# Kernel optimization log

Measured on AMD Instinct MI355X. Metric: run time of the kernel, lower is better.

Reference implementation:

```python
import jax, jax.numpy as jnp
import numpy as np

SR = 22050.0  # samplerate; nyquist = SR/2


def _conv1d(x, w, b, pad):
    # x: [B, Cin, T], w: [Cout, Cin, K]
    y = jax.lax.conv_general_dilated(x, w, (1,), [(pad, pad)],
                                     dimension_numbers=('NCH', 'OIH', 'NCH'))
    return y + b[None, :, None]


def _lrelu(x):
    return jnp.where(x >= 0, x, 0.2 * x)


def _lin_upsample(x, factor):
    # torch F.upsample(mode='linear', align_corners=False) ~ half-pixel linear resize
    B, C, T = x.shape
    return jax.image.resize(x, (B, C, T * factor), method='linear')


def _oscillator_bank(f, a, sr):
    # f, a: [B, n_osc, T] -> audio [B, T]
    f = jnp.clip(f, 20.0, sr / 2.0)
    phase = jnp.cumsum(f * (2.0 * np.pi / sr), axis=-1)  # cumulative phase integration
    return jnp.sum(jnp.sin(phase) * a, axis=1)


def _noise_bank2(mags, noise):
    # mags: [B, n_coeffs, n_frames] rfft magnitudes per frame; noise: [B, total_samples]
    B, n_coeffs, n_frames = mags.shape
    window = (n_coeffs - 1) * 2
    hop = window // 2
    total = hop * n_frames
    padded = jnp.pad(noise, ((0, 0), (0, hop)))           # [B, total + hop]
    blocks = padded.reshape(B, n_frames + 1, hop)
    frames = jnp.concatenate([blocks[:, :-1], blocks[:, 1:]], axis=-1)  # [B, n_frames, window]
    spec = jnp.fft.rfft(frames, axis=-1)                   # [B, n_frames, n_coeffs]
    spec = spec * mags.transpose(0, 2, 1)                  # filter white noise per frame
    filt = jnp.fft.irfft(spec, n=window, axis=-1)          # (torch normalized rfft/irfft scales cancel)
    out = jnp.zeros((B, hop * (n_frames + 1)), filt.dtype)
    out = out.at[:, :n_frames * hop].add(filt[..., :hop].reshape(B, -1))
    out = out.at[:, hop:].add(filt[..., hop:].reshape(B, -1))
    return out[:, :total].reshape(B, 1, total)


def _forward(x, noise, mw0, mb0, mw1, mb1, mw2, mb2, mw3, mb3, fw, fb,
             gw0, gb0, gw1, gb1, gw2, gb2, gw3, gb3, lw, lb,
             nw0, nb0, nw1, nb1, nw2, nb2, nw3, nb3, nlw, nlb):
    B, _, T = x.shape
    up = noise.shape[1] // T  # upsample_factor = output_size // input_size
    n_osc = fw.shape[0]

    # oscillator frequency ranges (constants, as in __init__)
    stops = np.geomspace(20.0, SR / 2.0, num=n_osc)
    diffs = np.diff(np.concatenate([[0.0], stops]))
    starts = jnp.asarray(stops - diffs, jnp.float32)[None, :, None]
    diffs_j = jnp.asarray(diffs, jnp.float32)[None, :, None]

    # loudness path (main2 -> loudness ** 2)
    h = x
    for w_, b_ in ((gw0, gb0), (gw1, gb1), (gw2, gb2), (gw3, gb3)):
        h = _lrelu(_conv1d(h, w_, b_, 1))
    loud = _conv1d(h, lw, lb, 1) ** 2  # [B, n_osc, T]

    # frequency path (main -> sigmoid -> map to [start, stop])
    h = x
    for w_, b_ in ((mw0, mb0), (mw1, mb1), (mw2, mb2), (mw3, mb3)):
        h = _lrelu(_conv1d(h, w_, b_, 1))
    f = starts + jax.nn.sigmoid(_conv1d(h, fw, fb, 1)) * diffs_j  # [B, n_osc, T]

    h = x
    for w_, b_ in ((nw0, nb0), (nw1, nb1), (nw2, nb2), (nw3, nb3)):
        h = jnp.repeat(h, 2, axis=-1)
        h = _lrelu(_conv1d(h, w_, b_, 3))
    n_l = _conv1d(h, nlw, nlb, 1) ** 2  # [B, 17, 1024]

    loud = _lin_upsample(loud, up)  # [B, n_osc, output_size]
    f = _lin_upsample(f, up)
    harmonic = _oscillator_bank(f, loud, SR).reshape(B, 1, -1)
    return harmonic + _noise_bank2(n_l, noise)


def setup_inputs() -> dict:
    key = jax.random.key(0)
    ks = jax.random.split(key, 40)
    B, Cin, T, c, n_osc, out_size = 16, 128, 64, 512, 128, 16384
    n_coeffs = out_size // 1024 + 1  # 17
    inp = {}
    inp['x'] = jax.random.normal(ks[0], (B, Cin, T), jnp.float32)
    inp['noise'] = jax.random.uniform(ks[1], (B, out_size), jnp.float32, minval=-1.0, maxval=1.0)
    specs = [('mw0', c, Cin, 3), ('mw1', c, c, 3), ('mw2', c, c, 3), ('mw3', c, c, 3), ('fw', n_osc, c, 3),
             ('gw0', c, Cin, 3), ('gw1', c, c, 3), ('gw2', c, c, 3), ('gw3', c, c, 3), ('lw', n_osc, c, 3),
             ('nw0', c, Cin, 7), ('nw1', c, c, 7), ('nw2', c, c, 7), ('nw3', c, c, 7), ('nlw', n_coeffs, c, 3)]
    for j, (nm, o, i, ksz) in enumerate(specs):
        kw, kb = jax.random.split(ks[2 + j])
        inp[nm] = jax.random.normal(kw, (o, i, ksz), jnp.float32) * (1.0 / np.sqrt(i * ksz))
        inp[nm.replace('w', 'b', 1)] = jax.random.normal(kb, (o,), jnp.float32) * 0.01
    return inp


def reference(x, noise, mw0, mb0, mw1, mb1, mw2, mb2, mw3, mb3, fw, fb,
              gw0, gb0, gw1, gb1, gw2, gb2, gw3, gb3, lw, lb,
              nw0, nb0, nw1, nb1, nw2, nb2, nw3, nb3, nlw, nlb):
    return _forward(x, noise, mw0, mb0, mw1, mb1, mw2, mb2, mw3, mb3, fw, fb,
                    gw0, gb0, gw1, gb1, gw2, gb2, gw3, gb3, lw, lb,
                    nw0, nb0, nw1, nb1, nw2, nb2, nw3, nb3, nlw, nlb)
```

## Files before the change

### kernel.cpp

```cpp
#include <hip/hip_runtime.h>
#include <math.h>

#define ACT_LRELU  0
#define ACT_SIGMAP 1
#define ACT_SQUARE 2

typedef __attribute__((ext_vector_type(8))) short v8s;
typedef __attribute__((ext_vector_type(4))) short v4s;
typedef __attribute__((ext_vector_type(16))) float f32x16;

static __device__ __forceinline__ float lrelu(float x) { return x >= 0.f ? x : 0.2f * x; }

static __device__ __forceinline__ short bf16rne(float x) {
  unsigned u = __float_as_uint(x);
  unsigned r = (u + 0x7FFFu + ((u >> 16) & 1u)) >> 16;
  return (short)r;
}
static __device__ __forceinline__ float bf16tof(short h) {
  return __uint_as_float(((unsigned)(unsigned short)h) << 16);
}
static __device__ __forceinline__ void split3(float v, short& h, short& l, short& q) {
  h = bf16rne(v); float r1 = v - bf16tof(h);
  l = bf16rne(r1); float r2 = r1 - bf16tof(l);
  q = bf16rne(r2);
}

__global__ void __launch_bounds__(256) prep_acts(
    const float* __restrict__ x, short* __restrict__ xm3)
{
  int e = blockIdx.x * 256 + threadIdx.x;
  if (e >= 131072) return;
  int b = e >> 13, rem = e & 8191, t = rem >> 7, ci = rem & 127;
  float v = x[((size_t)(b * 128) + ci) * 64 + t];
  short h, l, q; split3(v, h, l, q);
  size_t o = ((size_t)(b * 64) + t) * 128 + ci;
  xm3[0 * 131072 + o] = h;
  xm3[1 * 131072 + o] = l;
  xm3[2 * 131072 + o] = q;
}

__global__ void __launch_bounds__(256) prep_panels(
    const float* mw0, const float* mw1, const float* mw2, const float* mw3, const float* fw,
    const float* gw0, const float* gw1, const float* gw2, const float* gw3, const float* lw,
    short* __restrict__ mP, short* __restrict__ gP)
{
  int i = blockIdx.x * 256 + threadIdx.x;
  const int PER = 114688;
  if (i >= 2 * PER) return;
  int path = i >= PER ? 1 : 0;
  int r = i - path * PER;
  int layer, Cin, Cout; size_t poff;
  if (r < 8192)        { layer = 0;              Cin = 128; Cout = 512; poff = 0; }
  else if (r < 40960)  { layer = 1; r -= 8192;   Cin = 512; Cout = 512; poff = 589824; }
  else if (r < 73728)  { layer = 2; r -= 40960;  Cin = 512; Cout = 512; poff = 2949120; }
  else if (r < 106496) { layer = 3; r -= 73728;  Cin = 512; Cout = 512; poff = 5308416; }
  else                 { layer = 4; r -= 106496; Cin = 512; Cout = 128; poff = 7667712; }
  const float* Wm[5] = {mw0, mw1, mw2, mw3, fw};
  const float* Wg[5] = {gw0, gw1, gw2, gw3, lw};
  const float* W = path ? Wg[layer] : Wm[layer];
  short* P = (path ? gP : mP) + poff;
  const int nci8 = Cin >> 3;
  int co = r / nci8, ci = (r - co * nci8) * 8;
  const int K3 = 3 * Cin;
  const float* wp = W + (size_t)(co * Cin + ci) * 3;
  v8s hv[3], lv[3], qv[3];
#pragma unroll
  for (int j = 0; j < 8; ++j)
#pragma unroll
    for (int tap = 0; tap < 3; ++tap) {
      short h, l, q; split3(wp[j * 3 + tap], h, l, q);
      hv[tap][j] = h; lv[tap][j] = l; qv[tap][j] = q;
    }
#pragma unroll
  for (int tap = 0; tap < 3; ++tap) {
    size_t base = (size_t)co * K3 + tap * Cin + ci;
    *(v8s*)&P[(size_t)0 * Cout * K3 + base] = hv[tap];
    *(v8s*)&P[(size_t)1 * Cout * K3 + base] = lv[tap];
    *(v8s*)&P[(size_t)2 * Cout * K3 + base] = qv[tap];
  }
}

__global__ void __launch_bounds__(128, 2) conv_path_tap(
    const short* __restrict__ actM, const short* __restrict__ actG,
    const short* __restrict__ Pm, const short* __restrict__ Pg,
    float* __restrict__ partial, int Cin, int Cout, int psIn)
{
  const int mtiles = Cout >> 6;
  const int nblk = 2 * mtiles * 16 * 3;
  const int Q = nblk >> 3;
  int d = blockIdx.x;
  int idx = (d & 7) * Q + (d >> 3);
  int mt = idx % mtiles; int r = idx / mtiles;
  int nt = r & 15; r >>= 4;
  int tap = r % 3; int path = r / 3;

  const short* act = path ? actG : actM;
  const short* P   = path ? Pg : Pm;
  const int K3 = 3 * Cin;
  const int co0 = mt * 64;
  const int NT  = Cin >> 5;
  const int npl = path ? 2 : 3;

  const int tid = threadIdx.x;
  const int w = tid >> 6;
  const int l = tid & 63;

  __shared__ __align__(16) short Al[3][64 * 40];
  __shared__ __align__(16) short Bl[3][64 * 40];

  f32x16 acc[2] = {};
  v8s rA[3][2], rB[3][2];

  auto LOADA = [&](int t) {
    int ci0 = t << 5;
#pragma unroll
    for (int pl = 0; pl < 3; ++pl) {
      if (pl >= npl) break;
#pragma unroll
      for (int it = 0; it < 2; ++it) {
        int e = it * 128 + tid;
        int row = e >> 2, c8 = e & 3;
        rA[pl][it] = *(const v8s*)&P[(size_t)pl * Cout * K3 + (size_t)(co0 + row) * K3
                                     + tap * Cin + ci0 + c8 * 8];
      }
    }
  };
  auto LOADB = [&](int t) {
    int ci0 = t << 5;
#pragma unroll
    for (int pl = 0; pl < 3; ++pl) {
      if (pl >= npl) break;
#pragma unroll
      for (int it = 0; it < 2; ++it) {
        int e = it * 128 + tid;
        int n = e >> 2, c8 = e & 3;
        int trow = n + tap - 1;
        v8s vv = {};
        if (trow >= 0 && trow < 64)
          vv = *(const v8s*)&act[(size_t)pl * psIn + ((size_t)(nt * 64 + trow)) * Cin
                                 + ci0 + c8 * 8];
        rB[pl][it] = vv;
      }
    }
  };
  auto WRITE = [&]() {
#pragma unroll
    for (int pl = 0; pl < 3; ++pl) {
      if (pl >= npl) break;
#pragma unroll
      for (int it = 0; it < 2; ++it) {
        int e = it * 128 + tid;
        *(v8s*)&Al[pl][(e >> 2) * 40 + (e & 3) * 8] = rA[pl][it];
        *(v8s*)&Bl[pl][(e >> 2) * 40 + (e & 3) * 8] = rB[pl][it];
      }
    }
  };

  LOADA(0); LOADB(0);
  WRITE();
  __syncthreads();

  for (int t = 0; t < NT; ++t) {
    if (t + 1 < NT) { LOADA(t + 1); LOADB(t + 1); }
    const int lr = l & 31, lh = (l >> 5) * 8;
#pragma unroll
    for (int kk = 0; kk < 2; ++kk) {
      const int ao = (w * 32 + lr) * 40 + kk * 16 + lh;
      v8s a0 = *(const v8s*)&Al[0][ao];
      v8s a1 = *(const v8s*)&Al[1][ao];
#pragma unroll
      for (int fn = 0; fn < 2; ++fn) {
        const int bo = (fn * 32 + lr) * 40 + kk * 16 + lh;
        v8s b0 = *(const v8s*)&Bl[0][bo];
        v8s b1 = *(const v8s*)&Bl[1][bo];
        acc[fn] = __builtin_amdgcn_mfma_f32_32x32x16_bf16(a0, b0, acc[fn], 0, 0, 0);
        acc[fn] = __builtin_amdgcn_mfma_f32_32x32x16_bf16(a0, b1, acc[fn], 0, 0, 0);
        acc[fn] = __builtin_amdgcn_mfma_f32_32x32x16_bf16(a1, b0, acc[fn], 0, 0, 0);
        if (path == 0) {
          v8s a2 = *(const v8s*)&Al[2][ao];
          v8s b2 = *(const v8s*)&Bl[2][bo];
          acc[fn] = __builtin_amdgcn_mfma_f32_32x32x16_bf16(a1, b1, acc[fn], 0, 0, 0);
          acc[fn] = __builtin_amdgcn_mfma_f32_32x32x16_bf16(a0, b2, acc[fn], 0, 0, 0);
          acc[fn] = __builtin_amdgcn_mfma_f32_32x32x16_bf16(a2, b0, acc[fn], 0, 0, 0);
        }
      }
    }
    __syncthreads();
    if (t + 1 < NT) { WRITE(); __syncthreads(); }
  }

  const int hi4 = 4 * (l >> 5);
  const size_t pbase = (size_t)(tap * 2 + path) * 1024;
#pragma unroll
  for (int fn = 0; fn < 2; ++fn) {
    int gn = nt * 64 + fn * 32 + (l & 31);
#pragma unroll
    for (int q4 = 0; q4 < 4; ++q4) {
      int co = co0 + w * 32 + q4 * 8 + hi4;
      float4 v = {acc[fn][q4 * 4 + 0], acc[fn][q4 * 4 + 1],
                  acc[fn][q4 * 4 + 2], acc[fn][q4 * 4 + 3]};
      *(float4*)&partial[(pbase + gn) * Cout + co] = v;
    }
  }
}

__global__ void __launch_bounds__(256) finalize_lrelu(
    const float* __restrict__ partial,
    const float* __restrict__ BsM, const float* __restrict__ BsG,
    short* __restrict__ soutM, short* __restrict__ soutG)
{
  int e = blockIdx.x * 256 + threadIdx.x;
  int c4 = e & 127, gn = (e >> 7) & 1023, path = e >> 17;
  const float* Bs = path ? BsG : BsM;
  short* sout = path ? soutG : soutM;
  size_t base = ((size_t)(path) * 1024 + gn) * 512 + c4 * 4;
  const size_t TS = (size_t)2 * 1024 * 512;
  float4 s0 = *(const float4*)&partial[base];
  float4 s1 = *(const float4*)&partial[base + TS];
  float4 s2 = *(const float4*)&partial[base + 2 * TS];
  float4 bi = *(const float4*)&Bs[c4 * 4];
  const float* p0 = &s0.x; const float* p1 = &s1.x;
  const float* p2 = &s2.x; const float* pb = &bi.x;
  v4s h4, l4, q4v;
#pragma unroll
  for (int j = 0; j < 4; ++j) {
    float z = lrelu(p0[j] + p1[j] + p2[j] + pb[j]);
    short h, lo, qq; split3(z, h, lo, qq);
    h4[j] = h; l4[j] = lo; q4v[j] = qq;
  }
  size_t o = (size_t)gn * 512 + c4 * 4;
  *(v4s*)&sout[0 * 524288 + o] = h4;
  *(v4s*)&sout[1 * 524288 + o] = l4;
  *(v4s*)&sout[2 * 524288 + o] = q4v;
}

__global__ void __launch_bounds__(256) finalize_l5(
    const float* __restrict__ partial,
    const float* __restrict__ fb, const float* __restrict__ lb,
    float* __restrict__ fsm, float* __restrict__ lsm)
{
  __shared__ float bandS[2][128];
  int tid = threadIdx.x;
  if (tid < 128) {
    double lg = log(551.25);
    double stop  = 20.0 * exp(lg * (double)tid / 127.0);
    double start = (tid == 0) ? 0.0 : 20.0 * exp(lg * (double)(tid - 1) / 127.0);
    bandS[0][tid] = (float)start;
    bandS[1][tid] = (float)(stop - start);
  }
  __syncthreads();

  int e = blockIdx.x * 256 + tid;
  int c4 = e & 31, gn = (e >> 5) & 1023, path = e >> 15;
  size_t base = ((size_t)(path) * 1024 + gn) * 128 + c4 * 4;
  const size_t TS = (size_t)2 * 1024 * 128;
  float4 s0 = *(const float4*)&partial[base];
  float4 s1 = *(const float4*)&partial[base + TS];
  float4 s2 = *(const float4*)&partial[base + 2 * TS];
  float4 bi = *(const float4*)&((path ? lb : fb)[c4 * 4]);
  const float* p0 = &s0.x; const float* p1 = &s1.x;
  const float* p2 = &s2.x; const float* pb = &bi.x;
  int b = gn >> 6, t = gn & 63;
#pragma unroll
  for (int j = 0; j < 4; ++j) {
    int co = c4 * 4 + j;
    float z = p0[j] + p1[j] + p2[j] + pb[j];
    if (path == 0)
      fsm[((size_t)(b * 128) + co) * 64 + t] = bandS[0][co] + bandS[1][co] / (1.f + expf(-z));
    else
      lsm[((size_t)(b * 128) + co) * 64 + t] = z * z;
  }
}

__global__ void __launch_bounds__(256) fold_all(
    const float* __restrict__ nw0, const float* __restrict__ nw1,
    const float* __restrict__ nw2, const float* __restrict__ nw3,
    const float* __restrict__ nlw,
    short* __restrict__ E1, short* __restrict__ E2,
    short* __restrict__ E3, short* __restrict__ E4,
    short* __restrict__ Pnl)
{
  int i = blockIdx.x * 256 + threadIdx.x;
  if (i >= 106496) {
    if (i >= 108544) return;
    int idx = i - 106496;
    int co = idx >> 6, ci = (idx & 63) * 8;
    v8s hv[3], lv[3];
#pragma unroll
    for (int j = 0; j < 8; ++j)
#pragma unroll
      for (int tap = 0; tap < 3; ++tap) {
        float v = (co < 17) ? nlw[((size_t)(co * 512 + ci + j)) * 3 + tap] : 0.f;
        short h = bf16rne(v);
        hv[tap][j] = h;
        lv[tap][j] = bf16rne(v - bf16tof(h));
      }
#pragma unroll
    for (int tap = 0; tap < 3; ++tap) {
      *(v8s*)&Pnl[(size_t)(0 * 32 + co) * 1536 + tap * 512 + ci] = hv[tap];
      *(v8s*)&Pnl[(size_t)(1 * 32 + co) * 1536 + tap * 512 + ci] = lv[tap];
    }
    return;
  }
  const float* W; short* Ag; int Cin; int idx;
  if (i < 8192)        { W = nw0; Ag = E1; Cin = 128; idx = i; }
  else if (i < 40960)  { W = nw1; Ag = E2; Cin = 512; idx = i - 8192; }
  else if (i < 73728)  { W = nw2; Ag = E3; Cin = 512; idx = i - 40960; }
  else                 { W = nw3; Ag = E4; Cin = 512; idx = i - 73728; }
  const int nci8 = Cin >> 3;
  int co = idx / nci8, ci = (idx - co * nci8) * 8;
  const float* wp = W + (size_t)(co * Cin + ci) * 7;
  const int K = Cin * 4;
  v8s he[4], le[4], ho[4], lo4[4];
#pragma unroll
  for (int j = 0; j < 8; ++j) {
    const float* w = wp + j * 7;
    float fe[4] = {w[0],        w[1] + w[2], w[3] + w[4], w[5] + w[6]};
    float fo[4] = {w[0] + w[1], w[2] + w[3], w[4] + w[5], w[6]};
#pragma unroll
    for (int q = 0; q < 4; ++q) {
      short h1 = bf16rne(fe[q]);
      he[q][j] = h1; le[q][j] = bf16rne(fe[q] - bf16tof(h1));
      short h2 = bf16rne(fo[q]);
      ho[q][j] = h2; lo4[q][j] = bf16rne(fo[q] - bf16tof(h2));
    }
  }
#pragma unroll
  for (int q = 0; q < 4; ++q) {
    size_t kbase = (size_t)q * Cin + ci;
    *(v8s*)&Ag[((size_t)(0 * 512 + co)) * K + kbase] = he[q];
    *(v8s*)&Ag[((size_t)(1 * 512 + co)) * K + kbase] = le[q];
    *(v8s*)&Ag[((size_t)(2 * 512 + co)) * K + kbase] = ho[q];
    *(v8s*)&Ag[((size_t)(3 * 512 + co)) * K + kbase] = lo4[q];
  }
}

template<int MF, int BNS, int CIN>
__global__ void __launch_bounds__(256, 2) conv_noise(
    const short* __restrict__ actIn, const short* __restrict__ Ag,
    const float* __restrict__ Bs, short* __restrict__ actOut,
    int Sin, int psIn, int psOut)
{
  constexpr int NF   = BNS / 64;
  constexpr int BM   = MF * 64;
  constexpr int AITS = BM / 32;
  constexpr int BITS = BNS / 32;
  constexpr int K    = CIN * 4;
  constexpr int nci  = CIN / 64;
  constexpr int NT   = 4 * nci;
  const int mtiles = 512 / BM;
  const int stiles = Sin / BNS;
  const int nblk = mtiles * 2 * 16 * stiles;
  const int Q = nblk >> 3;
  int d = blockIdx.x;
  int idx = (d & 7) * Q + (d >> 3);
  int mt = idx % mtiles;
  int t1 = idx / mtiles;
  int par = t1 & 1;
  int rest = t1 >> 1;
  int st = rest % stiles;
  int b = rest / stiles;

  const int co0 = mt * BM;
  const int s0 = st * BNS;
  const int soff = par ? -1 : -2;

  const int tid = threadIdx.x;
  const int w = tid >> 6, wm = w & 1, wn = w >> 1;
  const int l = tid & 63;

  __shared__ __align__(16) short Al[2][BM * 72];
  __shared__ __align__(16) short Bl[2][BNS * 72];

  f32x16 acc[MF][NF] = {};
  v8s rA[2][AITS], rB[2][BITS];

  auto LOADA = [&](int t) {
    int q = t / nci, ci0 = (t % nci) << 6;
#pragma unroll
    for (int pl = 0; pl < 2; ++pl)
#pragma unroll
      for (int it = 0; it < AITS; ++it) {
        int e = it * 256 + tid;
        int row = e >> 3, c8 = e & 7;
        rA[pl][it] = *(const v8s*)&Ag[((size_t)((par * 2 + pl) * 512 + co0 + row)) * K
                                      + q * CIN + ci0 + c8 * 8];
      }
  };
  auto LOADB = [&](int t) {
    int q = t / nci, ci0 = (t % nci) << 6;
#pragma unroll
    for (int pl = 0; pl < 2; ++pl)
#pragma unroll
      for (int it = 0; it < BITS; ++it) {
        int e = it * 256 + tid;
        int n = e >> 3, c8 = e & 7;
        int srow = s0 + n + q + soff;
        v8s vv = {};
        if (srow >= 0 && srow < Sin)
          vv = *(const v8s*)&actIn[(size_t)pl * psIn + ((size_t)(b * Sin + srow)) * CIN
                                   + ci0 + c8 * 8];
        rB[pl][it] = vv;
      }
  };
  auto WRITE = [&]() {
#pragma unroll
    for (int pl = 0; pl < 2; ++pl) {
#pragma unroll
      for (int it = 0; it < AITS; ++it) {
        int e = it * 256 + tid;
        *(v8s*)&Al[pl][(e >> 3) * 72 + (e & 7) * 8] = rA[pl][it];
      }
#pragma unroll
      for (int it = 0; it < BITS; ++it) {
        int e = it * 256 + tid;
        *(v8s*)&Bl[pl][(e >> 3) * 72 + (e & 7) * 8] = rB[pl][it];
      }
    }
  };

  LOADA(0); LOADB(0);
  WRITE();
  __syncthreads();

  for (int t = 0; t < NT; ++t) {
    if (t + 1 < NT) { LOADA(t + 1); LOADB(t + 1); }
    const int lr = l & 31, lh = (l >> 5) * 8;
#pragma unroll
    for (int kk = 0; kk < 4; ++kk) {
      v8s ah[MF], al[MF], bh[NF], bl[NF];
#pragma unroll
      for (int fm = 0; fm < MF; ++fm) {
        int ab = (wm * (MF * 32) + fm * 32 + lr) * 72 + kk * 16 + lh;
        ah[fm] = *(const v8s*)&Al[0][ab];
        al[fm] = *(const v8s*)&Al[1][ab];
      }
#pragma unroll
      for (int fn = 0; fn < NF; ++fn) {
        int bb = (wn * (BNS / 2) + fn * 32 + lr) * 72 + kk * 16 + lh;
        bh[fn] = *(const v8s*)&Bl[0][bb];
        bl[fn] = *(const v8s*)&Bl[1][bb];
      }
#pragma unroll
      for (int fm = 0; fm < MF; ++fm)
#pragma unroll
        for (int fn = 0; fn < NF; ++fn) {
          acc[fm][fn] = __builtin_amdgcn_mfma_f32_32x32x16_bf16(ah[fm], bh[fn], acc[fm][fn], 0, 0, 0);
          acc[fm][fn] = __builtin_amdgcn_mfma_f32_32x32x16_bf16(ah[fm], bl[fn], acc[fm][fn], 0, 0, 0);
          acc[fm][fn] = __builtin_amdgcn_mfma_f32_32x32x16_bf16(al[fm], bh[fn], acc[fm][fn], 0, 0, 0);
        }
    }
    __syncthreads();
    if (t + 1 < NT) { WRITE(); __syncthreads(); }
  }

  const int hi4 = 4 * (l >> 5);
  const int T2 = 2 * Sin;
#pragma unroll
  for (int fm = 0; fm < MF; ++fm)
#pragma unroll
    for (int q4 = 0; q4 < 4; ++q4) {
      int co = co0 + wm * (MF * 32) + fm * 32 + q4 * 8 + hi4;
      float4 bia = *(const float4*)&Bs[co];
      const float* bp = &bia.x;
#pragma unroll
      for (int fn = 0; fn < NF; ++fn) {
        int s_l = wn * (BNS / 2) + fn * 32 + (l & 31);
        int t = 2 * (s0 + s_l) + par;
        v4s h4, l4;
#pragma unroll
        for (int j = 0; j < 4; ++j) {
          float z = lrelu(acc[fm][fn][q4 * 4 + j] + bp[j]);
          short h = bf16rne(z);
          h4[j] = h;
          l4[j] = bf16rne(z - bf16tof(h));
        }
        size_t o = ((size_t)(b * T2) + t) * 512 + co;
        *(v4s*)&actOut[0 * (size_t)psOut + o] = h4;
        *(v4s*)&actOut[1 * (size_t)psOut + o] = l4;
      }
    }
}

#define NL_PS4 8388608

__global__ void __launch_bounds__(128) conv_nl_mfma(
    const short* __restrict__ act, const short* __restrict__ Pnl,
    const float* __restrict__ Bs, float* __restrict__ outNl)
{
  const int bid = blockIdx.x;
  const int b = bid >> 4, t0 = (bid & 15) << 6;
  const int tid = threadIdx.x;
  const int w = tid >> 6;
  const int l = tid & 63;

  __shared__ __align__(16) short Al[2 * 3 * 32 * 72];
  __shared__ __align__(16) short Bl[2 * 66 * 72];

  f32x16 acc = {};

  for (int ci0 = 0; ci0 < 512; ci0 += 64) {
    for (int e = tid; e < 1536; e += 128) {
      int c8 = e & 7, row = e >> 3;
      int pl = row >= 96;
      int r2 = row - pl * 96;
      int tap = r2 >> 5, co = r2 & 31;
      v8s vv = *(const v8s*)&Pnl[(size_t)(pl * 32 + co) * 1536 + tap * 512 + ci0 + c8 * 8];
      *(v8s*)&Al[row * 72 + c8 * 8] = vv;
    }
    for (int e = tid; e < 1056; e += 128) {
      int c8 = e & 7, r = (e >> 3) % 66, pl = (e >> 3) / 66;
      int t = t0 + r - 1;
      v8s vv = {};
      if (t >= 0 && t < 1024)
        vv = *(const v8s*)&act[(size_t)pl * NL_PS4 + ((size_t)(b << 10) + t) * 512 + ci0 + c8 * 8];
      *(v8s*)&Bl[(pl * 66 + r) * 72 + c8 * 8] = vv;
    }
    __syncthreads();
    const int lr = l & 31, lh = (l >> 5) * 8;
#pragma unroll
    for (int kk = 0; kk < 4; ++kk)
#pragma unroll
      for (int tap = 0; tap < 3; ++tap) {
        v8s a_h = *(const v8s*)&Al[((0 * 3 + tap) * 32 + lr) * 72 + kk * 16 + lh];
        v8s a_l = *(const v8s*)&Al[((1 * 3 + tap) * 32 + lr) * 72 + kk * 16 + lh];
        int brow = w * 32 + lr + tap;
        v8s b_h = *(const v8s*)&Bl[(0 * 66 + brow) * 72 + kk * 16 + lh];
        v8s b_l = *(const v8s*)&Bl[(1 * 66 + brow) * 72 + kk * 16 + lh];
        acc = __builtin_amdgcn_mfma_f32_32x32x16_bf16(a_h, b_h, acc, 0, 0, 0);
        acc = __builtin_amdgcn_mfma_f32_32x32x16_bf16(a_h, b_l, acc, 0, 0, 0);
        acc = __builtin_amdgcn_mfma_f32_32x32x16_bf16(a_l, b_h, acc, 0, 0, 0);
      }
    __syncthreads();
  }

  const int t = t0 + w * 32 + (l & 31);
  const int hi4 = 4 * (l >> 5);
#pragma unroll
  for (int q4 = 0; q4 < 4; ++q4) {
#pragma unroll
    for (int j = 0; j < 4; ++j) {
      int co = q4 * 8 + hi4 + j;
      if (co < 17) {
        float z = acc[q4 * 4 + j] + Bs[co];
        outNl[((size_t)(b * 17) + co) * 1024 + t] = z * z;
      }
    }
  }
}

__global__ void __launch_bounds__(64) noise_filter(
    const float* __restrict__ noise, const float* __restrict__ mags,
    float* __restrict__ filt)
{
  __shared__ float ct[32], st[32];
  int tid = threadIdx.x;
  if (tid < 32) {
    double a = (double)tid * (3.14159265358979323846 / 16.0);
    ct[tid] = (float)cos(a);
    st[tid] = (float)sin(a);
  }
  __syncthreads();

  int fidx = blockIdx.x * 64 + tid;
  int b = fidx >> 10, i = fidx & 1023;

  float xv[32];
#pragma unroll
  for (int n = 0; n < 32; ++n) {
    int idx = i * 16 + n;
    xv[n] = (idx < 16384) ? noise[(size_t)b * 16384 + idx] : 0.f;
  }

  float Yr[17], Yi[17];
#pragma unroll
  for (int k = 0; k <= 16; ++k) {
    float xr = 0.f, xi = 0.f;
    int kk = 0;
#pragma unroll
    for (int n = 0; n < 32; ++n) {
      xr += xv[n] * ct[kk];
      xi -= xv[n] * st[kk];
      kk = (kk + k) & 31;
    }
    float m = mags[((size_t)b * 17 + k) * 1024 + i];
    Yr[k] = xr * m;
    Yi[k] = xi * m;
  }

  float* fo = filt + ((size_t)b * 1024 + i) * 32;
#pragma unroll
  for (int n = 0; n < 32; ++n) {
    float v = Yr[0] + ((n & 1) ? -Yr[16] : Yr[16]);
    int kk = n;
#pragma unroll
    for (int k = 1; k <= 15; ++k) {
      v += 2.f * (Yr[k] * ct[kk] - Yi[k] * st[kk]);
      kk = (kk + n) & 31;
    }
    fo[n] = v * (1.f / 32.f);
  }
}

static __device__ __forceinline__ int clamp64(int i) { return i < 0 ? 0 : (i > 63 ? 63 : i); }

__global__ void __launch_bounds__(256) osc_phase(
    const float* __restrict__ fsm, double* __restrict__ phaseBase)
{
  const int o = blockIdx.x, b = blockIdx.y;
  const float* frow = fsm + (size_t)(b * 128 + o) * 64;
  const int c = threadIdx.x;

  const float ic0 = ((float)(c * 64) - 127.5f) * (1.0f / 256.0f);
  const int ilo = (int)floorf(ic0);
  float f0 = frow[clamp64(ilo)], f1 = frow[clamp64(ilo + 1)], f2 = frow[clamp64(ilo + 2)];

  double local = 0.0;
#pragma unroll 8
  for (int j = 0; j < 64; ++j) {
    float ic = ic0 + (float)j * (1.0f / 256.0f);
    float fl = floorf(ic);
    float w  = ic - fl;
    bool hi = ((int)fl) > ilo;
    float fa = hi ? f1 : f0;
    float fb = hi ? f2 : f1;
    float f = fa * (1.f - w) + fb * w;
    f = fminf(fmaxf(f, 20.f), 11025.f);
    local += (double)f;
  }
  local *= (1.0 / 22050.0);

  __shared__ double ps[256];
  ps[c] = local;
  __syncthreads();
  for (int off = 1; off < 256; off <<= 1) {
    double v = (c >= off) ? ps[c - off] : 0.0;
    __syncthreads();
    ps[c] += v;
    __syncthreads();
  }
  phaseBase[(size_t)(b * 128 + o) * 256 + c] = ps[c] - local;
}

__global__ void __launch_bounds__(128) osc_sum(
    const float* __restrict__ fsm, const float* __restrict__ lsm,
    const double* __restrict__ phaseBase, const float* __restrict__ filt,
    float* __restrict__ out)
{
  const int c = blockIdx.x, b = blockIdx.y;
  const int tid = threadIdx.x;
  __shared__ float contrib[128][65];
  __shared__ float part[2][64];
  const int o = tid;
  const float* frow = fsm + (size_t)(b * 128 + o) * 64;
  const float* arow = lsm + (size_t)(b * 128 + o) * 64;

  double pb = phaseBase[(size_t)(b * 128 + o) * 256 + c];
  float fb0 = (float)(pb - floor(pb));

  const float ic0 = ((float)(c * 64) - 127.5f) * (1.0f / 256.0f);
  const int ilo = (int)floorf(ic0);
  float f0 = frow[clamp64(ilo)], f1 = frow[clamp64(ilo + 1)], f2 = frow[clamp64(ilo + 2)];
  float a0 = arow[clamp64(ilo)], a1 = arow[clamp64(ilo + 1)], a2 = arow[clamp64(ilo + 2)];

  float rel = 0.f, comp = 0.f;
#pragma unroll 8
  for (int j = 0; j < 64; ++j) {
    float ic = ic0 + (float)j * (1.0f / 256.0f);
    float fl = floorf(ic);
    float w  = ic - fl;
    bool hi = ((int)fl) > ilo;
    float fa = hi ? f1 : f0;
    float fb = hi ? f2 : f1;
    float f = fa * (1.f - w) + fb * w;
    f = fminf(fmaxf(f, 20.f), 11025.f);
    float y = f * (1.0f / 22050.0f) - comp;
    float t = rel + y;
    comp = (t - rel) - y;
    rel = t;
    float tot = fb0 + rel;
    float frac = tot - floorf(tot);
    float s = sinpif(2.f * frac);
    float aa = hi ? a1 : a0;
    float ab = hi ? a2 : a1;
    float am = aa * (1.f - w) + ab * w;
    contrib[o][j] = s * am;
  }
  __syncthreads();
  int half = tid >> 6, tl = tid & 63;
  float sum = 0.f;
  for (int oo = 0; oo < 64; ++oo) sum += contrib[half * 64 + oo][tl];
  part[half][tl] = sum;
  __syncthreads();
  if (tid < 64) {
    int t = c * 64 + tid;
    float v = part[0][tid] + part[1][tid];
    int i0 = t >> 4, r = t & 15;
    v += filt[((size_t)(b << 10) + i0) * 32 + r];
    if (i0 > 0) v += filt[((size_t)(b << 10) + i0 - 1) * 32 + 16 + r];
    out[(size_t)b * 16384 + t] = v;
  }
}

extern "C" void kernel_launch(void* const* d_in, const int* in_sizes, int n_in,
                              void* d_out, int out_size, void* d_ws, size_t ws_size,
                              hipStream_t stream)
{
  (void)in_sizes; (void)n_in; (void)out_size; (void)ws_size;

  const float* x     = (const float*)d_in[0];
  const float* noise = (const float*)d_in[1];
  const float* mw0 = (const float*)d_in[2];  const float* mb0 = (const float*)d_in[3];
  const float* mw1 = (const float*)d_in[4];  const float* mb1 = (const float*)d_in[5];
  const float* mw2 = (const float*)d_in[6];  const float* mb2 = (const float*)d_in[7];
  const float* mw3 = (const float*)d_in[8];  const float* mb3 = (const float*)d_in[9];
  const float* fw  = (const float*)d_in[10]; const float* fb  = (const float*)d_in[11];
  const float* gw0 = (const float*)d_in[12]; const float* gb0 = (const float*)d_in[13];
  const float* gw1 = (const float*)d_in[14]; const float* gb1 = (const float*)d_in[15];
  const float* gw2 = (const float*)d_in[16]; const float* gb2 = (const float*)d_in[17];
  const float* gw3 = (const float*)d_in[18]; const float* gb3 = (const float*)d_in[19];
  const float* lw  = (const float*)d_in[20]; const float* lb  = (const float*)d_in[21];
  const float* nw0 = (const float*)d_in[22]; const float* nb0 = (const float*)d_in[23];
  const float* nw1 = (const float*)d_in[24]; const float* nb1 = (const float*)d_in[25];
  const float* nw2 = (const float*)d_in[26]; const float* nb2 = (const float*)d_in[27];
  const float* nw3 = (const float*)d_in[28]; const float* nb3 = (const float*)d_in[29];
  const float* nlw = (const float*)d_in[30]; const float* nlb = (const float*)d_in[31];

  char* W8 = (char*)d_ws;
  short* mP  = (short*)(W8 + 0);
  short* gP  = (short*)(W8 + 16515072);
  short* hm0 = (short*)(W8 + 33030144);
  short* hm1 = (short*)(W8 + 36175872);
  short* hg0 = (short*)(W8 + 39321600);
  short* hg1 = (short*)(W8 + 42467328);
  float* partial = (float*)(W8 + 45613056);
  short* xm3 = (short*)(W8 + 58720256);
  float* fsm = (float*)(W8 + 59506688);
  float* lsm = (float*)(W8 + 60030976);
  short* Pnl = (short*)(W8 + 60555264);

  short* E4  = (short*)(W8 + 0);
  short* E3  = (short*)(W8 + 33554432);
  short* E2  = (short*)(W8 + 41943040);
  short* E1  = (short*)(W8 + 50331648);
  short* l1out = (short*)(W8 + 52428800);
  short* l2out = (short*)(W8 + 25165824);
  short* l3out = (short*)(W8 + 8388608);
  short* l4act = (short*)(W8 + 25165824);

  float* nl   = (float*)(W8 + 0);
  float* filt = (float*)(W8 + 1114112);
  double* phaseBase = (double*)(W8 + 4194304);

  float* out = (float*)d_out;

  const int PS_X = 131072;
  const int PS_H = 524288;

  prep_acts<<<512, 256, 0, stream>>>(x, xm3);
  prep_panels<<<896, 256, 0, stream>>>(mw0, mw1, mw2, mw3, fw,
                                       gw0, gw1, gw2, gw3, lw, mP, gP);

  conv_path_tap<<<768, 128, 0, stream>>>(xm3, xm3, mP + 0, gP + 0, partial, 128, 512, PS_X);
  finalize_lrelu<<<1024, 256, 0, stream>>>(partial, mb0, gb0, hm0, hg0);
  conv_path_tap<<<768, 128, 0, stream>>>(hm0, hg0, mP + 589824, gP + 589824, partial, 512, 512, PS_H);
  finalize_lrelu<<<1024, 256, 0, stream>>>(partial, mb1, gb1, hm1, hg1);
  conv_path_tap<<<768, 128, 0, stream>>>(hm1, hg1, mP + 2949120, gP + 2949120, partial, 512, 512, PS_H);
  finalize_lrelu<<<1024, 256, 0, stream>>>(partial, mb2, gb2, hm0, hg0);
  conv_path_tap<<<768, 128, 0, stream>>>(hm0, hg0, mP + 5308416, gP + 5308416, partial, 512, 512, PS_H);
  finalize_lrelu<<<1024, 256, 0, stream>>>(partial, mb3, gb3, hm1, hg1);
  conv_path_tap<<<192, 128, 0, stream>>>(hm1, hg1, mP + 7667712, gP + 7667712, partial, 512, 128, PS_H);
  finalize_l5<<<256, 256, 0, stream>>>(partial, fb, lb, fsm, lsm);

  fold_all<<<424, 256, 0, stream>>>(nw0, nw1, nw2, nw3, nlw, E1, E2, E3, E4, Pnl);
  conv_noise<1, 64, 128><<<256, 256, 0, stream>>>(xm3, E1, nb0, l1out, 64, PS_X, 1048576);
  conv_noise<2, 64, 512><<<256, 256, 0, stream>>>(l1out, E2, nb1, l2out, 128, 1048576, 2097152);
  conv_noise<2, 128, 512><<<256, 256, 0, stream>>>(l2out, E3, nb2, l3out, 256, 2097152, 4194304);
  conv_noise<2, 128, 512><<<512, 256, 0, stream>>>(l3out, E4, nb3, l4act, 512, 4194304, 8388608);

  conv_nl_mfma<<<256, 128, 0, stream>>>(l4act, Pnl, nlb, nl);

  noise_filter<<<256, 64, 0, stream>>>(noise, nl, filt);

  osc_phase<<<dim3(128, 16), 256, 0, stream>>>(fsm, phaseBase);
  osc_sum<<<dim3(256, 16), 128, 0, stream>>>(fsm, lsm, phaseBase, filt, out);
}
```

Measured before the change: 535.7 us.

## Reuse shifted activation slab across taps in conv_noise and fuse noise filter

conv_noise now loads one activation slab of BNS+3 rows per 64-channel chunk and reuses it for all four taps by offsetting the LDS row index, instead of reloading the B tile for every tap. This cuts global loads and LDS writes for the activation operand. In exchange, A-panel loads are pipelined per tap, and extra branches are added on the last tap. Separately, the noise-layer conv is fused with the per-frame FFT filter, so magnitudes stay in shared memory instead of round-tripping through global memory, though only half the threads do the filter work. The conv_path_tap loop guards are also rewritten from break to if.

```diff
diff --git a/kernel.cpp b/kernel.cpp
--- a/kernel.cpp
+++ b/kernel.cpp
@@ -114,46 +114,43 @@
   auto LOADA = [&](int t) {
     int ci0 = t << 5;
 #pragma unroll
-    for (int pl = 0; pl < 3; ++pl) {
-      if (pl >= npl) break;
-#pragma unroll
-      for (int it = 0; it < 2; ++it) {
-        int e = it * 128 + tid;
-        int row = e >> 2, c8 = e & 3;
-        rA[pl][it] = *(const v8s*)&P[(size_t)pl * Cout * K3 + (size_t)(co0 + row) * K3
-                                     + tap * Cin + ci0 + c8 * 8];
-      }
-    }
+    for (int pl = 0; pl < 3; ++pl)
+      if (pl < npl)
+#pragma unroll
+        for (int it = 0; it < 2; ++it) {
+          int e = it * 128 + tid;
+          int row = e >> 2, c8 = e & 3;
+          rA[pl][it] = *(const v8s*)&P[(size_t)pl * Cout * K3 + (size_t)(co0 + row) * K3
+                                       + tap * Cin + ci0 + c8 * 8];
+        }
   };
   auto LOADB = [&](int t) {
     int ci0 = t << 5;
 #pragma unroll
-    for (int pl = 0; pl < 3; ++pl) {
-      if (pl >= npl) break;
-#pragma unroll
-      for (int it = 0; it < 2; ++it) {
-        int e = it * 128 + tid;
-        int n = e >> 2, c8 = e & 3;
-        int trow = n + tap - 1;
-        v8s vv = {};
-        if (trow >= 0 && trow < 64)
-          vv = *(const v8s*)&act[(size_t)pl * psIn + ((size_t)(nt * 64 + trow)) * Cin
-                                 + ci0 + c8 * 8];
-        rB[pl][it] = vv;
-      }
-    }
+    for (int pl = 0; pl < 3; ++pl)
+      if (pl < npl)
+#pragma unroll
+        for (int it = 0; it < 2; ++it) {
+          int e = it * 128 + tid;
+          int n = e >> 2, c8 = e & 3;
+          int trow = n + tap - 1;
+          v8s vv = {};
+          if (trow >= 0 && trow < 64)
+            vv = *(const v8s*)&act[(size_t)pl * psIn + ((size_t)(nt * 64 + trow)) * Cin
+                                   + ci0 + c8 * 8];
+          rB[pl][it] = vv;
+        }
   };
   auto WRITE = [&]() {
 #pragma unroll
-    for (int pl = 0; pl < 3; ++pl) {
-      if (pl >= npl) break;
-#pragma unroll
-      for (int it = 0; it < 2; ++it) {
-        int e = it * 128 + tid;
-        *(v8s*)&Al[pl][(e >> 2) * 40 + (e & 3) * 8] = rA[pl][it];
-        *(v8s*)&Bl[pl][(e >> 2) * 40 + (e & 3) * 8] = rB[pl][it];
-      }
-    }
+    for (int pl = 0; pl < 3; ++pl)
+      if (pl < npl)
+#pragma unroll
+        for (int it = 0; it < 2; ++it) {
+          int e = it * 128 + tid;
+          *(v8s*)&Al[pl][(e >> 2) * 40 + (e & 3) * 8] = rA[pl][it];
+          *(v8s*)&Bl[pl][(e >> 2) * 40 + (e & 3) * 8] = rB[pl][it];
+        }
   };
 
   LOADA(0); LOADB(0);
@@ -344,10 +341,10 @@
   constexpr int NF   = BNS / 64;
   constexpr int BM   = MF * 64;
   constexpr int AITS = BM / 32;
-  constexpr int BITS = BNS / 32;
+  constexpr int SLAB = BNS + 3;
+  constexpr int BSL  = (2 * SLAB * 8 + 255) / 256;
   constexpr int K    = CIN * 4;
   constexpr int nci  = CIN / 64;
-  constexpr int NT   = 4 * nci;
   const int mtiles = 512 / BM;
   const int stiles = Sin / BNS;
   const int nblk = mtiles * 2 * 16 * stiles;
@@ -370,13 +367,13 @@
   const int l = tid & 63;
 
   __shared__ __align__(16) short Al[2][BM * 72];
-  __shared__ __align__(16) short Bl[2][BNS * 72];
+  __shared__ __align__(16) short Bl[2][SLAB * 72];
 
   f32x16 acc[MF][NF] = {};
-  v8s rA[2][AITS], rB[2][BITS];
-
-  auto LOADA = [&](int t) {
-    int q = t / nci, ci0 = (t % nci) << 6;
+  v8s rA[2][AITS];
+  v8s rBS[BSL];
+
+  auto LOADA = [&](int q, int ci0) {
 #pragma unroll
     for (int pl = 0; pl < 2; ++pl)
 #pragma unroll
@@ -387,71 +384,88 @@
                                       + q * CIN + ci0 + c8 * 8];
       }
   };
-  auto LOADB = [&](int t) {
-    int q = t / nci, ci0 = (t % nci) << 6;
+  auto WRITEA = [&]() {
 #pragma unroll
     for (int pl = 0; pl < 2; ++pl)
 #pragma unroll
-      for (int it = 0; it < BITS; ++it) {
+      for (int it = 0; it < AITS; ++it) {
         int e = it * 256 + tid;
-        int n = e >> 3, c8 = e & 7;
-        int srow = s0 + n + q + soff;
-        v8s vv = {};
+        *(v8s*)&Al[pl][(e >> 3) * 72 + (e & 7) * 8] = rA[pl][it];
+      }
+  };
+  auto LOADBS = [&](int ci0) {
+#pragma unroll
+    for (int it = 0; it < BSL; ++it) {
+      int e = it * 256 + tid;
+      v8s vv = {};
+      if (e < 2 * SLAB * 8) {
+        int r3 = e >> 3, c8 = e & 7;
+        int pl = r3 / SLAB, row = r3 - pl * SLAB;
+        int srow = s0 + soff + row;
         if (srow >= 0 && srow < Sin)
           vv = *(const v8s*)&actIn[(size_t)pl * psIn + ((size_t)(b * Sin + srow)) * CIN
                                    + ci0 + c8 * 8];
-        rB[pl][it] = vv;
-      }
+      }
+      rBS[it] = vv;
+    }
   };
-  auto WRITE = [&]() {
-#pragma unroll
-    for (int pl = 0; pl < 2; ++pl) {
-#pragma unroll
-      for (int it = 0; it < AITS; ++it) {
-        int e = it * 256 + tid;
-        *(v8s*)&Al[pl][(e >> 3) * 72 + (e & 7) * 8] = rA[pl][it];
-      }
-#pragma unroll
-      for (int it = 0; it < BITS; ++it) {
-        int e = it * 256 + tid;
-        *(v8s*)&Bl[pl][(e >> 3) * 72 + (e & 7) * 8] = rB[pl][it];
+  auto WRITEBS = [&]() {
+#pragma unroll
+    for (int it = 0; it < BSL; ++it) {
+      int e = it * 256 + tid;
+      if (e < 2 * SLAB * 8) {
+        int r3 = e >> 3, c8 = e & 7;
+        int pl = r3 / SLAB, row = r3 - pl * SLAB;
+        *(v8s*)&Bl[pl][row * 72 + c8 * 8] = rBS[it];
       }
     }
   };
 
-  LOADA(0); LOADB(0);
-  WRITE();
+  LOADBS(0); LOADA(0, 0);
+  WRITEBS(); WRITEA();
   __syncthreads();
 
-  for (int t = 0; t < NT; ++t) {
-    if (t + 1 < NT) { LOADA(t + 1); LOADB(t + 1); }
-    const int lr = l & 31, lh = (l >> 5) * 8;
-#pragma unroll
-    for (int kk = 0; kk < 4; ++kk) {
-      v8s ah[MF], al[MF], bh[NF], bl[NF];
-#pragma unroll
-      for (int fm = 0; fm < MF; ++fm) {
-        int ab = (wm * (MF * 32) + fm * 32 + lr) * 72 + kk * 16 + lh;
-        ah[fm] = *(const v8s*)&Al[0][ab];
-        al[fm] = *(const v8s*)&Al[1][ab];
-      }
-#pragma unroll
-      for (int fn = 0; fn < NF; ++fn) {
-        int bb = (wn * (BNS / 2) + fn * 32 + lr) * 72 + kk * 16 + lh;
-        bh[fn] = *(const v8s*)&Bl[0][bb];
-        bl[fn] = *(const v8s*)&Bl[1][bb];
-      }
-#pragma unroll
-      for (int fm = 0; fm < MF; ++fm)
+  for (int ci = 0; ci < nci; ++ci) {
+    const int ci0 = ci << 6;
+#pragma unroll
+    for (int q = 0; q < 4; ++q) {
+      const bool lastq = (q == 3);
+      const bool lastall = lastq && (ci == nci - 1);
+      if (!lastq)        LOADA(q + 1, ci0);
+      else if (!lastall) { LOADBS(ci0 + 64); LOADA(0, ci0 + 64); }
+
+      const int lr = l & 31, lh = (l >> 5) * 8;
+#pragma unroll
+      for (int kk = 0; kk < 4; ++kk) {
+        v8s ah[MF], al[MF], bh[NF], bl[NF];
+#pragma unroll
+        for (int fm = 0; fm < MF; ++fm) {
+          int ab = (wm * (MF * 32) + fm * 32 + lr) * 72 + kk * 16 + lh;
+          ah[fm] = *(const v8s*)&Al[0][ab];
+          al[fm] = *(const v8s*)&Al[1][ab];
+        }
 #pragma unroll
         for (int fn = 0; fn < NF; ++fn) {
-          acc[fm][fn] = __builtin_amdgcn_mfma_f32_32x32x16_bf16(ah[fm], bh[fn], acc[fm][fn], 0, 0, 0);
-          acc[fm][fn] = __builtin_amdgcn_mfma_f32_32x32x16_bf16(ah[fm], bl[fn], acc[fm][fn], 0, 0, 0);
-          acc[fm][fn] = __builtin_amdgcn_mfma_f32_32x32x16_bf16(al[fm], bh[fn], acc[fm][fn], 0, 0, 0);
+          int bb = (wn * (BNS / 2) + fn * 32 + lr + q) * 72 + kk * 16 + lh;
+          bh[fn] = *(const v8s*)&Bl[0][bb];
+          bl[fn] = *(const v8s*)&Bl[1][bb];
         }
-    }
-    __syncthreads();
-    if (t + 1 < NT) { WRITE(); __syncthreads(); }
+#pragma unroll
+        for (int fm = 0; fm < MF; ++fm)
+#pragma unroll
+          for (int fn = 0; fn < NF; ++fn) {
+            acc[fm][fn] = __builtin_amdgcn_mfma_f32_32x32x16_bf16(ah[fm], bh[fn], acc[fm][fn], 0, 0, 0);
+            acc[fm][fn] = __builtin_amdgcn_mfma_f32_32x32x16_bf16(ah[fm], bl[fn], acc[fm][fn], 0, 0, 0);
+            acc[fm][fn] = __builtin_amdgcn_mfma_f32_32x32x16_bf16(al[fm], bh[fn], acc[fm][fn], 0, 0, 0);
+          }
+      }
+      __syncthreads();
+      if (!lastall) {
+        if (!lastq) WRITEA();
+        else { WRITEBS(); WRITEA(); }
+        __syncthreads();
+      }
+    }
   }
 
   const int hi4 = 4 * (l >> 5);
@@ -484,9 +498,10 @@
 
 #define NL_PS4 8388608
 
-__global__ void __launch_bounds__(128) conv_nl_mfma(
+__global__ void __launch_bounds__(128) conv_nl_filter(
     const short* __restrict__ act, const short* __restrict__ Pnl,
-    const float* __restrict__ Bs, float* __restrict__ outNl)
+    const float* __restrict__ Bs, const float* __restrict__ noise,
+    float* __restrict__ filt)
 {
   const int bid = blockIdx.x;
   const int b = bid >> 4, t0 = (bid & 15) << 6;
@@ -496,6 +511,14 @@
 
   __shared__ __align__(16) short Al[2 * 3 * 32 * 72];
   __shared__ __align__(16) short Bl[2 * 66 * 72];
+  __shared__ float magS[64][20];
+  __shared__ float ctS[32], stS[32];
+
+  if (tid < 32) {
+    double a = (double)tid * (3.14159265358979323846 / 16.0);
+    ctS[tid] = (float)cos(a);
+    stS[tid] = (float)sin(a);
+  }
 
   f32x16 acc = {};
 
@@ -534,71 +557,55 @@
     __syncthreads();
   }
 
-  const int t = t0 + w * 32 + (l & 31);
+  const int t_loc = w * 32 + (l & 31);
   const int hi4 = 4 * (l >> 5);
 #pragma unroll
-  for (int q4 = 0; q4 < 4; ++q4) {
+  for (int q4 = 0; q4 < 4; ++q4)
 #pragma unroll
     for (int j = 0; j < 4; ++j) {
       int co = q4 * 8 + hi4 + j;
       if (co < 17) {
         float z = acc[q4 * 4 + j] + Bs[co];
-        outNl[((size_t)(b * 17) + co) * 1024 + t] = z * z;
-      }
-    }
-  }
-}
-
-__global__ void __launch_bounds__(64) noise_filter(
-    const float* __restrict__ noise, const float* __restrict__ mags,
-    float* __restrict__ filt)
-{
-  __shared__ float ct[32], st[32];
-  int tid = threadIdx.x;
-  if (tid < 32) {
-    double a = (double)tid * (3.14159265358979323846 / 16.0);
-    ct[tid] = (float)cos(a);
-    st[tid] = (float)sin(a);
-  }
+        magS[t_loc][co] = z * z;
+      }
+    }
   __syncthreads();
 
-  int fidx = blockIdx.x * 64 + tid;
-  int b = fidx >> 10, i = fidx & 1023;
-
-  float xv[32];
-#pragma unroll
-  for (int n = 0; n < 32; ++n) {
-    int idx = i * 16 + n;
-    xv[n] = (idx < 16384) ? noise[(size_t)b * 16384 + idx] : 0.f;
-  }
-
-  float Yr[17], Yi[17];
-#pragma unroll
-  for (int k = 0; k <= 16; ++k) {
-    float xr = 0.f, xi = 0.f;
-    int kk = 0;
+  if (tid < 64) {
+    int i = t0 + tid;
+    float xv[32];
 #pragma unroll
     for (int n = 0; n < 32; ++n) {
-      xr += xv[n] * ct[kk];
-      xi -= xv[n] * st[kk];
-      kk = (kk + k) & 31;
-    }
-    float m = mags[((size_t)b * 17 + k) * 1024 + i];
-    Yr[k] = xr * m;
-    Yi[k] = xi * m;
-  }
-
-  float* fo = filt + ((size_t)b * 1024 + i) * 32;
-#pragma unroll
-  for (int n = 0; n < 32; ++n) {
-    float v = Yr[0] + ((n & 1) ? -Yr[16] : Yr[16]);
-    int kk = n;
-#pragma unroll
-    for (int k = 1; k <= 15; ++k) {
-      v += 2.f * (Yr[k] * ct[kk] - Yi[k] * st[kk]);
-      kk = (kk + n) & 31;
-    }
-    fo[n] = v * (1.f / 32.f);
+      int idx = i * 16 + n;
+      xv[n] = (idx < 16384) ? noise[(size_t)b * 16384 + idx] : 0.f;
+    }
+    float Yr[17], Yi[17];
+#pragma unroll
+    for (int k = 0; k <= 16; ++k) {
+      float xr = 0.f, xi = 0.f;
+      int kk = 0;
+#pragma unroll
+      for (int n = 0; n < 32; ++n) {
+        xr += xv[n] * ctS[kk];
+        xi -= xv[n] * stS[kk];
+        kk = (kk + k) & 31;
+      }
+      float m = magS[tid][k];
+      Yr[k] = xr * m;
+      Yi[k] = xi * m;
+    }
+    float* fo = filt + ((size_t)(b << 10) + i) * 32;
+#pragma unroll
+    for (int n = 0; n < 32; ++n) {
+      float v = Yr[0] + ((n & 1) ? -Yr[16] : Yr[16]);
+      int kk = n;
+#pragma unroll
+      for (int k = 1; k <= 15; ++k) {
+        v += 2.f * (Yr[k] * ctS[kk] - Yi[k] * stS[kk]);
+        kk = (kk + n) & 31;
+      }
+      fo[n] = v * (1.f / 32.f);
+    }
   }
 }
 
@@ -748,7 +755,6 @@
   short* l3out = (short*)(W8 + 8388608);
   short* l4act = (short*)(W8 + 25165824);
 
-  float* nl   = (float*)(W8 + 0);
   float* filt = (float*)(W8 + 1114112);
   double* phaseBase = (double*)(W8 + 4194304);
 
@@ -778,9 +784,7 @@
   conv_noise<2, 128, 512><<<256, 256, 0, stream>>>(l2out, E3, nb2, l3out, 256, 2097152, 4194304);
   conv_noise<2, 128, 512><<<512, 256, 0, stream>>>(l3out, E4, nb3, l4act, 512, 4194304, 8388608);
 
-  conv_nl_mfma<<<256, 128, 0, stream>>>(l4act, Pnl, nlb, nl);
-
-  noise_filter<<<256, 64, 0, stream>>>(noise, nl, filt);
+  conv_nl_filter<<<256, 128, 0, stream>>>(l4act, Pnl, nlb, noise, filt);
 
   osc_phase<<<dim3(128, 16), 256, 0, stream>>>(fsm, phaseBase);
   osc_sum<<<dim3(256, 16), 128, 0, stream>>>(fsm, lsm, phaseBase, filt, out);
```

Measured after the change: 514.9 us. 3.9% less time.
